# Performance work log

Measured on AMD Instinct MI355X. Metric: run time of the kernel, lower is better.

## Reference

```python
import jax, jax.numpy as jnp
import numpy as np

N, D = 50000, 1000
FH1, FH2 = 256, 128
GH1, GH2, H = 64, 30, 3
NC = 10
E = 800000
BN_EPS = 1e-5


def setup_inputs() -> dict:
    key = jax.random.key(0)
    ks = iter(jax.random.split(key, 48))
    nk = lambda: next(ks)
    r = lambda *s: jax.random.normal(nk(), s, jnp.float32) * 0.05
    g = lambda n: 1.0 + jax.random.normal(nk(), (n,), jnp.float32) * 0.01
    return dict(
        x=jax.random.normal(nk(), (N, D), jnp.float32),
        edge_index=jax.random.randint(nk(), (2, E), 0, N, dtype=jnp.int32),
        enc_w1=r(D, FH1), enc_b1=r(FH1), enc_g1=g(FH1), enc_bt1=r(FH1),
        enc_w2=r(FH1, FH2), enc_b2=r(FH2), enc_g2=g(FH2), enc_bt2=r(FH2),
        gat1_w=r(FH2, H * GH1), gat1_asrc=r(H, GH1), gat1_adst=r(H, GH1), gat1_b=r(H * GH1),
        gat2_w=r(H * GH1, GH2), gat2_asrc=r(1, GH2), gat2_adst=r(1, GH2), gat2_b=r(GH2),
        gat3_w=r(H * GH1, GH2), gat3_asrc=r(1, GH2), gat3_adst=r(1, GH2), gat3_b=r(GH2),
        dec_w1=r(GH2, FH2), dec_b1=r(FH2), dec_g1=g(FH2), dec_bt1=r(FH2),
        dec_w2=r(FH2, FH1), dec_b2=r(FH1), dec_g2=g(FH1), dec_bt2=r(FH1),
        dec_w3=r(FH1, D), dec_b3=r(D),
        clu_w1=r(GH2, FH2), clu_b1=r(FH2), clu_g1=g(FH2), clu_bt1=r(FH2),
        clu_w2=r(FH2, NC), clu_b2=r(NC),
    )


def _bn_elu(h, w, b, gm, bt):
    # Linear -> BatchNorm1d (batch stats) -> ELU; dropout is identity at eval
    h = h @ w + b
    m = h.mean(0)
    v = h.var(0)
    return jax.nn.elu(gm * (h - m) * jax.lax.rsqrt(v + BN_EPS) + bt)


def _gat(h, src, dst, n, w, a_src, a_dst, b, heads, oc, concat):
    # PyG GATConv: per-head linear, edge-wise LeakyReLU(0.2) scores,
    # softmax over incoming edges of each dst node, weighted scatter-sum.
    hh = (h @ w).reshape(n, heads, oc)            # [N,H,C]
    s_src = jnp.sum(hh * a_src, -1)               # [N,H]
    s_dst = jnp.sum(hh * a_dst, -1)               # [N,H]
    e = jax.nn.leaky_relu(s_src[src] + s_dst[dst], negative_slope=0.2)  # [E,H]
    m = jax.ops.segment_max(e, dst, num_segments=n)
    p = jnp.exp(e - m[dst])
    denom = jax.ops.segment_sum(p, dst, num_segments=n)
    alpha = p / denom[dst]                        # [E,H]
    msg = hh[src] * alpha[..., None]              # [E,H,C]
    out = jax.ops.segment_sum(msg, dst, num_segments=n)
    out = out.reshape(n, heads * oc) if concat else out.mean(1)
    return out + b


def reference(x, edge_index,
              enc_w1, enc_b1, enc_g1, enc_bt1, enc_w2, enc_b2, enc_g2, enc_bt2,
              gat1_w, gat1_asrc, gat1_adst, gat1_b,
              gat2_w, gat2_asrc, gat2_adst, gat2_b,
              gat3_w, gat3_asrc, gat3_adst, gat3_b,
              dec_w1, dec_b1, dec_g1, dec_bt1, dec_w2, dec_b2, dec_g2, dec_bt2, dec_w3, dec_b3,
              clu_w1, clu_b1, clu_g1, clu_bt1, clu_w2, clu_b2):
    n = x.shape[0]
    loops = jnp.arange(n, dtype=edge_index.dtype)  # GATConv add_self_loops=True
    src = jnp.concatenate([edge_index[0], loops])
    dst = jnp.concatenate([edge_index[1], loops])

    h = _bn_elu(x, enc_w1, enc_b1, enc_g1, enc_bt1)
    h = _bn_elu(h, enc_w2, enc_b2, enc_g2, enc_bt2)
    h = jax.nn.relu(_gat(h, src, dst, n, gat1_w, gat1_asrc, gat1_adst, gat1_b, H, GH1, True))
    mu = _gat(h, src, dst, n, gat2_w, gat2_asrc, gat2_adst, gat2_b, 1, GH2, False)
    logvar = _gat(h, src, dst, n, gat3_w, gat3_asrc, gat3_adst, gat3_b, 1, GH2, False)
    z = mu  # eval-mode reparameterize returns mu

    d = _bn_elu(z, dec_w1, dec_b1, dec_g1, dec_bt1)
    d = _bn_elu(d, dec_w2, dec_b2, dec_g2, dec_bt2)
    x_rec = d @ dec_w3 + dec_b3

    c = _bn_elu(z, clu_w1, clu_b1, clu_g1, clu_bt1)
    pred = jax.nn.softmax(c @ clu_w2 + clu_b2, axis=1)
    return (pred, x_rec, z, mu, logvar)
```

## Files before the change

### kernel.cpp

```cpp
#include <hip/hip_runtime.h>
#include <hip/hip_bf16.h>

typedef short short8 __attribute__((ext_vector_type(8)));
typedef short short4v __attribute__((ext_vector_type(4)));
typedef float f32x4 __attribute__((ext_vector_type(4)));

static __device__ __forceinline__ short f2bf(float f){
  __hip_bfloat16 h = __float2bfloat16(f);
  return __builtin_bit_cast(short, h);
}
static __device__ __forceinline__ float b2f(short s){
  unsigned int u = ((unsigned int)(unsigned short)s) << 16;
  return __builtin_bit_cast(float, u);
}
static __device__ __forceinline__ float lrelu(float x){ return x > 0.f ? x : 0.2f*x; }
static __device__ __forceinline__ float eluf(float x){ return x > 0.f ? x : (__expf(x)-1.f); }
static __device__ __forceinline__ int imin(int a,int b){ return a<b?a:b; }

typedef const __attribute__((address_space(1))) void as1_void;
typedef __attribute__((address_space(3))) void as3_void;
static __device__ __forceinline__ void gload16(const void* g, void* l){
  __builtin_amdgcn_global_load_lds((as1_void*)g, (as3_void*)l, 16, 0, 0);
}
template<int NN> __device__ __forceinline__ void wait_vm(){
  if constexpr (NN==0) asm volatile("s_waitcnt vmcnt(0)" ::: "memory");
  else if constexpr (NN==3) asm volatile("s_waitcnt vmcnt(3)" ::: "memory");
  else if constexpr (NN==4) asm volatile("s_waitcnt vmcnt(4)" ::: "memory");
  else if constexpr (NN==6) asm volatile("s_waitcnt vmcnt(6)" ::: "memory");
  else if constexpr (NN==8) asm volatile("s_waitcnt vmcnt(8)" ::: "memory");
}

__global__ __launch_bounds__(256) void cvt_x(const float* __restrict__ x, short* __restrict__ xb, int M){
  int row = blockIdx.x*2 + (threadIdx.x>>7);
  int c8  = (threadIdx.x&127)*8;
  if (row >= M || c8 >= 1000) return;
  const float* p = x + (size_t)row*1000 + c8;
  float4 f0 = *(const float4*)p, f1 = *(const float4*)(p+4);
  short8 o;
  o[0]=f2bf(f0.x);o[1]=f2bf(f0.y);o[2]=f2bf(f0.z);o[3]=f2bf(f0.w);
  o[4]=f2bf(f1.x);o[5]=f2bf(f1.y);o[6]=f2bf(f1.z);o[7]=f2bf(f1.w);
  *(short8*)&xb[(size_t)row*1000 + c8] = o;
}

template<int BN, bool OBF16, bool CSTATS>
__global__ __launch_bounds__(256) void gemm_g(
    const short* __restrict__ A, int lda, const short* __restrict__ Bt, int ldb,
    void* __restrict__ Cv, const float* __restrict__ bias,
    float* __restrict__ ssum, float* __restrict__ ssq,
    int M, int N, int K, int ldc)
{
  constexpr int BM = 128, BK = 32, GPR = 4;
  constexpr int WN = BN/2, FM = 4, FN = WN/16;
  constexpr int AI = (BM*GPR)/(4*64);
  constexpr int BI_T = (BN*GPR)/64;
  constexpr bool BDUP = (BI_T < 4);
  constexpr int BI = BDUP ? BI_T : BI_T/4;
  constexpr int LPT = AI + BI;
  constexpr int TS = (BM+BN)*BK;
  __shared__ short lds[4][TS];

  const int tid = threadIdx.x, wid = tid>>6, lane = tid&63;
  const int wm = wid>>1, wn = wid&1;
  const int bm = blockIdx.x*BM, bn = blockIdx.y*BN;
  const int lr = lane&15, lg = lane>>4;
  const int nt = (K + BK - 1)/BK;

  f32x4 acc[FM][FN] = {};

  auto STAGE = [&](int t){
    int buf = t & 3, k0 = t*BK;
    #pragma unroll
    for (int i=0;i<AI;i++){
      int ci = wid*AI + i;
      int c = ci*64 + lane;
      int row = c>>2, g = c&3;
      int gr = imin(bm+row, M-1);
      const short* src = A + (size_t)gr*lda + k0 + ((g ^ (row&3))<<3);
      gload16(src, &lds[buf][ci*512]);
    }
    #pragma unroll
    for (int i=0;i<BI;i++){
      int bi = BDUP ? i : wid*BI + i;
      int c = bi*64 + lane;
      int row = c>>2, g = c&3;
      const short* src = Bt + (size_t)(bn+row)*ldb + k0 + ((g ^ (row&3))<<3);
      gload16(src, &lds[buf][BM*BK + bi*512]);
    }
  };

  for (int s=0; s<3 && s<nt; ++s) STAGE(s);

  for (int t=0; t<nt; ++t){
    int newer = imin(nt, t+3) - t - 1;
    if (newer >= 2) wait_vm<2*LPT>();
    else if (newer == 1) wait_vm<LPT>();
    else wait_vm<0>();
    __builtin_amdgcn_s_barrier();
    __builtin_amdgcn_sched_barrier(0);
    if (t+3 < nt) STAGE(t+3);
    int buf = t & 3;
    short8 af[FM], bf[FN];
    #pragma unroll
    for (int m=0;m<FM;m++){
      int r = wm*64 + m*16 + lr;
      af[m] = *(short8*)&lds[buf][r*BK + ((lg ^ (r&3))<<3)];
    }
    #pragma unroll
    for (int n=0;n<FN;n++){
      int r = wn*WN + n*16 + lr;
      bf[n] = *(short8*)&lds[buf][BM*BK + r*BK + ((lg ^ (r&3))<<3)];
    }
    #pragma unroll
    for (int m=0;m<FM;m++)
      #pragma unroll
      for (int n=0;n<FN;n++)
        acc[m][n] = __builtin_amdgcn_mfma_f32_16x16x32_bf16(af[m], bf[n], acc[m][n], 0, 0, 0);
  }

  #pragma unroll
  for (int m=0;m<FM;m++)
    #pragma unroll
    for (int n=0;n<FN;n++)
      #pragma unroll
      for (int q=0;q<4;q++){
        int row = bm + wm*64 + m*16 + lg*4 + q;
        int col = bn + wn*WN + n*16 + lr;
        if (row < M && col < N){
          float v = acc[m][n][q];
          if (bias) v += bias[col];
          if (OBF16) ((short*)Cv)[(size_t)row*ldc + col] = f2bf(v);
          else       ((float*)Cv)[(size_t)row*ldc + col] = v;
        }
      }
  if (CSTATS){
    #pragma unroll
    for (int n=0;n<FN;n++){
      float s = 0.f, q2 = 0.f;
      #pragma unroll
      for (int m=0;m<FM;m++)
        #pragma unroll
        for (int q=0;q<4;q++){
          int row = bm + wm*64 + m*16 + lg*4 + q;
          if (row < M){ float v = acc[m][n][q]; s += v; q2 += v*v; }
        }
      s  += __shfl_xor(s, 16);  s += __shfl_xor(s, 32);
      q2 += __shfl_xor(q2, 16); q2 += __shfl_xor(q2, 32);
      if (lg == 0){
        int col = bn + wn*WN + n*16 + lr;
        atomicAdd(&ssum[col], s);
        atomicAdd(&ssq[col],  q2);
      }
    }
  }
}

struct WEnt { const float* src; short* dst; int K, N, KP, NR; };
struct WTab { WEnt e[10]; };
__global__ __launch_bounds__(256) void wtrans_all(WTab tab){
  WEnt w = tab.e[blockIdx.y];
  int gid = blockIdx.x*256 + threadIdx.x;
  if (gid >= w.NR * w.KP) return;
  int n = gid / w.KP, k = gid - n*w.KP;
  float v = (k < w.K && n < w.N) ? w.src[(size_t)k*w.N + n] : 0.f;
  w.dst[gid] = f2bf(v);
}

template<int C>
__global__ __launch_bounds__(256) void bn_elu_apply2(const float* __restrict__ H, short* __restrict__ O,
    int M, float invM,
    const float* __restrict__ ssum, const float* __restrict__ ssq,
    const float* __restrict__ g, const float* __restrict__ bt){
  __shared__ float sc[C], sh[C];
  for (int c = threadIdx.x; c < C; c += 256){
    float mn  = ssum[c]*invM;
    float var = ssq[c]*invM - mn*mn;
    float s = g[c]*rsqrtf(var + 1e-5f);
    sc[c] = s; sh[c] = bt[c] - mn*s;
  }
  __syncthreads();
  int total4 = M*(C/4);
  for (int i = blockIdx.x*256+threadIdx.x; i < total4; i += gridDim.x*256){
    float4 v = ((const float4*)H)[i];
    int cb = (i*4) & (C-1);
    short4v o;
    o[0] = f2bf(eluf(v.x*sc[cb+0]+sh[cb+0]));
    o[1] = f2bf(eluf(v.y*sc[cb+1]+sh[cb+1]));
    o[2] = f2bf(eluf(v.z*sc[cb+2]+sh[cb+2]));
    o[3] = f2bf(eluf(v.w*sc[cb+3]+sh[cb+3]));
    ((short4v*)O)[i] = o;
  }
}

__global__ __launch_bounds__(256) void bn_elu_split(const float* __restrict__ H,
    short* __restrict__ Od, short* __restrict__ Oc, int M, float invM,
    const float* __restrict__ ssum, const float* __restrict__ ssq,
    const float* __restrict__ gd, const float* __restrict__ btd,
    const float* __restrict__ gc, const float* __restrict__ btc){
  __shared__ float sc[256], sh[256];
  {
    int c = threadIdx.x;
    float mn  = ssum[c]*invM;
    float var = ssq[c]*invM - mn*mn;
    float gg = (c<128) ? gd[c] : gc[c-128];
    float bb = (c<128) ? btd[c] : btc[c-128];
    float s = gg*rsqrtf(var + 1e-5f);
    sc[c] = s; sh[c] = bb - mn*s;
  }
  __syncthreads();
  int total4 = M*64;
  for (int i = blockIdx.x*256+threadIdx.x; i < total4; i += gridDim.x*256){
    float4 v = ((const float4*)H)[i];
    int cb = (i*4) & 255;
    short4v o;
    o[0] = f2bf(eluf(v.x*sc[cb+0]+sh[cb+0]));
    o[1] = f2bf(eluf(v.y*sc[cb+1]+sh[cb+1]));
    o[2] = f2bf(eluf(v.z*sc[cb+2]+sh[cb+2]));
    o[3] = f2bf(eluf(v.w*sc[cb+3]+sh[cb+3]));
    int row = i>>6;
    short* O = (cb < 128) ? Od : Oc;
    *(short4v*)&O[(size_t)row*128 + (cb&127)] = o;
  }
}

__global__ void hist_kernel(const int* __restrict__ d, int E, int* __restrict__ deg){
  int i = blockIdx.x*256 + threadIdx.x;
  if (i < E) atomicAdd(&deg[d[i]], 1);
}
__global__ __launch_bounds__(256) void scan1(const int* __restrict__ deg, int* __restrict__ offs,
                                             int* __restrict__ bsum, int n){
  __shared__ int sm[256];
  int tid = threadIdx.x;
  int base = blockIdx.x*1024 + tid*4;
  int v0 = base+0<n ? deg[base+0] : 0;
  int v1 = base+1<n ? deg[base+1] : 0;
  int v2 = base+2<n ? deg[base+2] : 0;
  int v3 = base+3<n ? deg[base+3] : 0;
  int ts = v0+v1+v2+v3;
  sm[tid] = ts;
  __syncthreads();
  #pragma unroll
  for (int d=1; d<256; d<<=1){
    int t = (tid>=d) ? sm[tid-d] : 0;
    __syncthreads();
    sm[tid] += t;
    __syncthreads();
  }
  int ex = sm[tid] - ts;
  if (base+0<n) offs[base+0] = ex;
  if (base+1<n) offs[base+1] = ex+v0;
  if (base+2<n) offs[base+2] = ex+v0+v1;
  if (base+3<n) offs[base+3] = ex+v0+v1+v2;
  if (tid==255) bsum[blockIdx.x] = sm[255];
}
__global__ __launch_bounds__(256) void scan3(int* __restrict__ offs, const int* __restrict__ bsum,
                      int* __restrict__ cursor, int n, int total){
  __shared__ int base_sm;
  int tgt = blockIdx.x >> 2;
  if (threadIdx.x < 64){
    int j = threadIdx.x;
    int v = (j < tgt) ? bsum[j] : 0;
    #pragma unroll
    for (int d=32; d; d>>=1) v += __shfl_xor(v, d);
    if (j == 0) base_sm = v;
  }
  __syncthreads();
  int i = blockIdx.x*256 + threadIdx.x;
  if (i < n){ int v = offs[i] + base_sm; offs[i]=v; cursor[i]=v; }
  if (i == 0) offs[n] = total;
}
__global__ void scatter_kernel(const int* __restrict__ s, const int* __restrict__ d, int E,
                               int* __restrict__ cursor, int* __restrict__ csr){
  int i = blockIdx.x*256 + threadIdx.x;
  if (i < E){ int pos = atomicAdd(&cursor[d[i]], 1); csr[pos] = s[i]; }
}

__global__ __launch_bounds__(256) void gat1_scores_bf(const short* __restrict__ hh,
    const float* __restrict__ as, const float* __restrict__ ad,
    float* __restrict__ ss, float* __restrict__ sd, int n){
  int w = threadIdx.x >> 6, lane = threadIdx.x & 63;
  int row = blockIdx.x*4 + w;
  if (row >= n) return;
  const short* hr = hh + (size_t)row*192;
  float ps[3], pd[3];
  #pragma unroll
  for (int h=0; h<3; h++){
    float v = b2f(hr[h*64 + lane]);
    ps[h] = v * as[h*64+lane];
    pd[h] = v * ad[h*64+lane];
  }
  #pragma unroll
  for (int m=32; m; m>>=1){
    #pragma unroll
    for (int h=0;h<3;h++){ ps[h] += __shfl_xor(ps[h], m); pd[h] += __shfl_xor(pd[h], m); }
  }
  if (lane == 0){
    #pragma unroll
    for (int h=0;h<3;h++){ ss[row*3+h]=ps[h]; sd[row*3+h]=pd[h]; }
  }
}

__global__ __launch_bounds__(256) void gat1_gather_bf(const int* __restrict__ offs, const int* __restrict__ csr,
    const short* __restrict__ hh, const float* __restrict__ ss, const float* __restrict__ sd,
    const float* __restrict__ bias, short* __restrict__ out, int n){
  int w = threadIdx.x >> 6, lane = threadIdx.x & 63;
  int dst = blockIdx.x*4 + w;
  if (dst >= n) return;
  float sd0 = sd[dst*3+0], sd1 = sd[dst*3+1], sd2 = sd[dst*3+2];
  float p0 = __expf(lrelu(ss[dst*3+0]+sd0));
  float p1 = __expf(lrelu(ss[dst*3+1]+sd1));
  float p2 = __expf(lrelu(ss[dst*3+2]+sd2));
  const short* hr = hh + (size_t)dst*192;
  float a0 = p0*b2f(hr[lane]), a1 = p1*b2f(hr[64+lane]), a2 = p2*b2f(hr[128+lane]);
  float d0 = p0, d1 = p1, d2 = p2;
  int p = offs[dst], pe = offs[dst+1];
  for (; p+4 <= pe; p += 4){
    int s0=csr[p], s1=csr[p+1], s2=csr[p+2], s3=csr[p+3];
    float e00=ss[s0*3+0], e01=ss[s0*3+1], e02=ss[s0*3+2];
    float e10=ss[s1*3+0], e11=ss[s1*3+1], e12=ss[s1*3+2];
    float e20=ss[s2*3+0], e21=ss[s2*3+1], e22=ss[s2*3+2];
    float e30=ss[s3*3+0], e31=ss[s3*3+1], e32=ss[s3*3+2];
    const short* r0 = hh + (size_t)s0*192;
    const short* r1 = hh + (size_t)s1*192;
    const short* r2 = hh + (size_t)s2*192;
    const short* r3 = hh + (size_t)s3*192;
    float v00=b2f(r0[lane]), v01=b2f(r0[64+lane]), v02=b2f(r0[128+lane]);
    float v10=b2f(r1[lane]), v11=b2f(r1[64+lane]), v12=b2f(r1[128+lane]);
    float v20=b2f(r2[lane]), v21=b2f(r2[64+lane]), v22=b2f(r2[128+lane]);
    float v30=b2f(r3[lane]), v31=b2f(r3[64+lane]), v32=b2f(r3[128+lane]);
    float q00=__expf(lrelu(e00+sd0)), q01=__expf(lrelu(e01+sd1)), q02=__expf(lrelu(e02+sd2));
    float q10=__expf(lrelu(e10+sd0)), q11=__expf(lrelu(e11+sd1)), q12=__expf(lrelu(e12+sd2));
    float q20=__expf(lrelu(e20+sd0)), q21=__expf(lrelu(e21+sd1)), q22=__expf(lrelu(e22+sd2));
    float q30=__expf(lrelu(e30+sd0)), q31=__expf(lrelu(e31+sd1)), q32=__expf(lrelu(e32+sd2));
    a0 += q00*v00 + q10*v10 + q20*v20 + q30*v30;
    a1 += q01*v01 + q11*v11 + q21*v21 + q31*v31;
    a2 += q02*v02 + q12*v12 + q22*v22 + q32*v32;
    d0 += q00+q10+q20+q30;
    d1 += q01+q11+q21+q31;
    d2 += q02+q12+q22+q32;
  }
  for (; p < pe; ++p){
    int src = csr[p];
    float q0 = __expf(lrelu(ss[src*3+0]+sd0));
    float q1 = __expf(lrelu(ss[src*3+1]+sd1));
    float q2 = __expf(lrelu(ss[src*3+2]+sd2));
    const short* sr = hh + (size_t)src*192;
    a0 += q0*b2f(sr[lane]); a1 += q1*b2f(sr[64+lane]); a2 += q2*b2f(sr[128+lane]);
    d0 += q0; d1 += q1; d2 += q2;
  }
  float v0 = a0/d0 + bias[lane];
  float v1 = a1/d1 + bias[64+lane];
  float v2 = a2/d2 + bias[128+lane];
  short* orow = out + (size_t)dst*192;
  orow[lane]      = f2bf(v0 > 0.f ? v0 : 0.f);
  orow[64+lane]   = f2bf(v1 > 0.f ? v1 : 0.f);
  orow[128+lane]  = f2bf(v2 > 0.f ? v2 : 0.f);
}

__global__ __launch_bounds__(256) void gat23_scores(const float* __restrict__ hh23,
    const float* __restrict__ a2s, const float* __restrict__ a2d,
    const float* __restrict__ a3s, const float* __restrict__ a3d,
    float* __restrict__ s2s, float* __restrict__ s2d, float* __restrict__ s3s, float* __restrict__ s3d, int n){
  int w = threadIdx.x >> 6, lane = threadIdx.x & 63;
  int row = blockIdx.x*4 + w;
  if (row >= n) return;
  float p[4] = {0.f,0.f,0.f,0.f};
  if (lane < 30){
    float v2 = hh23[(size_t)row*64+lane], v3 = hh23[(size_t)row*64+32+lane];
    p[0]=v2*a2s[lane]; p[1]=v2*a2d[lane]; p[2]=v3*a3s[lane]; p[3]=v3*a3d[lane];
  }
  #pragma unroll
  for (int m=32; m; m>>=1){
    #pragma unroll
    for (int j=0;j<4;j++) p[j] += __shfl_xor(p[j], m);
  }
  if (lane == 0){ s2s[row]=p[0]; s2d[row]=p[1]; s3s[row]=p[2]; s3d[row]=p[3]; }
}

__global__ __launch_bounds__(256) void gat23_gather(const int* __restrict__ offs, const int* __restrict__ csr,
    const float* __restrict__ hh23,
    const float* __restrict__ s2s, const float* __restrict__ s2d,
    const float* __restrict__ s3s, const float* __restrict__ s3d,
    const float* __restrict__ b2, const float* __restrict__ b3,
    float* __restrict__ zs, float* __restrict__ mus, float* __restrict__ lvs,
    short* __restrict__ zbf, int n){
  int w = threadIdx.x >> 6, lane = threadIdx.x & 63;
  int dst = blockIdx.x*4 + w;
  if (dst >= n) return;
  bool lo = lane < 32;
  int c = lane & 31;
  bool valid = c < 30;
  float sdA = s2d[dst], sdB = s3d[dst];
  float sdx = lo ? sdA : sdB;
  const float* ssx = lo ? s2s : s3s;
  float p2 = __expf(lrelu(s2s[dst]+sdA));
  float p3 = __expf(lrelu(s3s[dst]+sdB));
  float val = valid ? hh23[(size_t)dst*64+lane] : 0.f;
  float acc = (lo ? p2 : p3) * val;
  float den2 = p2, den3 = p3;
  int p = offs[dst], pe = offs[dst+1];
  for (; p+4 <= pe; p += 4){
    int s0=csr[p], s1=csr[p+1], s2i=csr[p+2], s3i=csr[p+3];
    float eA0=ssx[s0], eA1=ssx[s1], eA2=ssx[s2i], eA3=ssx[s3i];
    float f20=s2s[s0], f21=s2s[s1], f22=s2s[s2i], f23=s2s[s3i];
    float f30=s3s[s0], f31=s3s[s1], f32=s3s[s2i], f33=s3s[s3i];
    float v0 = valid ? hh23[(size_t)s0*64+lane] : 0.f;
    float v1 = valid ? hh23[(size_t)s1*64+lane] : 0.f;
    float v2 = valid ? hh23[(size_t)s2i*64+lane] : 0.f;
    float v3 = valid ? hh23[(size_t)s3i*64+lane] : 0.f;
    float qx0=__expf(lrelu(eA0+sdx)), qx1=__expf(lrelu(eA1+sdx));
    float qx2=__expf(lrelu(eA2+sdx)), qx3=__expf(lrelu(eA3+sdx));
    acc += qx0*v0 + qx1*v1 + qx2*v2 + qx3*v3;
    den2 += __expf(lrelu(f20+sdA)) + __expf(lrelu(f21+sdA)) + __expf(lrelu(f22+sdA)) + __expf(lrelu(f23+sdA));
    den3 += __expf(lrelu(f30+sdB)) + __expf(lrelu(f31+sdB)) + __expf(lrelu(f32+sdB)) + __expf(lrelu(f33+sdB));
  }
  for (; p < pe; ++p){
    int src = csr[p];
    float q2 = __expf(lrelu(s2s[src]+sdA));
    float q3 = __expf(lrelu(s3s[src]+sdB));
    float v = valid ? hh23[(size_t)src*64+lane] : 0.f;
    acc += (lo ? q2 : q3) * v;
    den2 += q2; den3 += q3;
  }
  if (lo){
    if (valid){
      float v = acc/den2 + b2[c];
      zs[(size_t)dst*30+c]  = v;
      mus[(size_t)dst*30+c] = v;
      zbf[(size_t)dst*32+c] = f2bf(v);
    } else {
      zbf[(size_t)dst*32+c] = 0;
    }
  } else if (valid){
    lvs[(size_t)dst*30+c] = acc/den3 + b3[c];
  }
}

__global__ __launch_bounds__(256) void softmax10(const float* __restrict__ in, float* __restrict__ out, int n){
  int row = blockIdx.x*256 + threadIdx.x;
  if (row >= n) return;
  const float* r = in + (size_t)row*10;
  float m = r[0];
  #pragma unroll
  for (int j=1;j<10;j++) m = fmaxf(m, r[j]);
  float e[10], s = 0.f;
  #pragma unroll
  for (int j=0;j<10;j++){ e[j] = __expf(r[j]-m); s += e[j]; }
  float inv = 1.f/s;
  float* o = out + (size_t)row*10;
  #pragma unroll
  for (int j=0;j<10;j++) o[j] = e[j]*inv;
}

static inline int cdiv(int a, int b){ return (a + b - 1) / b; }

extern "C" void kernel_launch(void* const* d_in, const int* in_sizes, int n_in,
                              void* d_out, int out_size, void* d_ws, size_t ws_size,
                              hipStream_t stream)
{
  const float* x        = (const float*)d_in[0];
  const int*   ei       = (const int*)  d_in[1];
  const float* enc_w1   = (const float*)d_in[2];
  const float* enc_g1   = (const float*)d_in[4];
  const float* enc_bt1  = (const float*)d_in[5];
  const float* enc_w2   = (const float*)d_in[6];
  const float* enc_g2   = (const float*)d_in[8];
  const float* enc_bt2  = (const float*)d_in[9];
  const float* gat1_w   = (const float*)d_in[10];
  const float* gat1_as  = (const float*)d_in[11];
  const float* gat1_ad  = (const float*)d_in[12];
  const float* gat1_b   = (const float*)d_in[13];
  const float* gat2_w   = (const float*)d_in[14];
  const float* gat2_as  = (const float*)d_in[15];
  const float* gat2_ad  = (const float*)d_in[16];
  const float* gat2_b   = (const float*)d_in[17];
  const float* gat3_w   = (const float*)d_in[18];
  const float* gat3_as  = (const float*)d_in[19];
  const float* gat3_ad  = (const float*)d_in[20];
  const float* gat3_b   = (const float*)d_in[21];
  const float* dec_w1   = (const float*)d_in[22];
  const float* dec_g1   = (const float*)d_in[24];
  const float* dec_bt1  = (const float*)d_in[25];
  const float* dec_w2   = (const float*)d_in[26];
  const float* dec_g2   = (const float*)d_in[28];
  const float* dec_bt2  = (const float*)d_in[29];
  const float* dec_w3   = (const float*)d_in[30];
  const float* dec_b3   = (const float*)d_in[31];
  const float* clu_w1   = (const float*)d_in[32];
  const float* clu_g1   = (const float*)d_in[34];
  const float* clu_bt1  = (const float*)d_in[35];
  const float* clu_w2   = (const float*)d_in[36];
  const float* clu_b2   = (const float*)d_in[37];

  const int N = in_sizes[0] / 1000;
  const int E = in_sizes[1] / 2;
  const int* e_src = ei;
  const int* e_dst = ei + E;
  const float invN = 1.f/(float)N;

  float* out  = (float*)d_out;
  float* pred = out;
  float* xrec = out + (size_t)N*10;
  float* zs   = xrec + (size_t)N*1000;
  float* mus  = zs  + (size_t)N*30;
  float* lvs  = mus + (size_t)N*30;

  char* ws = (char*)d_ws;
  size_t off = 0;
  auto alloc = [&](size_t bytes)->char*{
    char* p = ws + off;
    off = (off + bytes + 255) & ~(size_t)255;
    return p;
  };
  short* t_enc1  = (short*)alloc(256*1024*2);
  short* t_enc2  = (short*)alloc(128*256*2);
  short* t_gat1  = (short*)alloc(192*128*2);
  short* t_gat23 = (short*)alloc(64*192*2);
  short* t_dc1   = (short*)alloc(256*32*2);
  short* t_dec2  = (short*)alloc(256*128*2);
  short* t_dec3  = (short*)alloc(1024*256*2);
  short* t_clu2  = (short*)alloc(32*128*2);
  float* h1f  = (float*)alloc((size_t)N*256*4);
  short* h1b  = (short*)alloc((size_t)N*256*2);
  float* h2f  = (float*)alloc((size_t)N*128*4);
  short* h2b  = (short*)alloc((size_t)N*128*2);
  short* hh1b = (short*)alloc((size_t)N*192*2);
  short* h3b  = (short*)alloc((size_t)N*192*2);
  float* hh23f= (float*)alloc((size_t)N*64*4);
  short* zbf  = (short*)alloc((size_t)N*32*2);
  float* ss1  = (float*)alloc((size_t)N*3*4);
  float* sd1  = (float*)alloc((size_t)N*3*4);
  float* s2s  = (float*)alloc((size_t)N*4);
  float* s2d  = (float*)alloc((size_t)N*4);
  float* s3s  = (float*)alloc((size_t)N*4);
  float* s3d  = (float*)alloc((size_t)N*4);
  float* stats= (float*)alloc(2048*4);
  int*   deg  = (int*)alloc((size_t)(N+1)*4);
  int*   offs = (int*)alloc((size_t)(N+1)*4);
  int*   curp = (int*)alloc((size_t)(N+1)*4);
  int*   bsum = (int*)alloc(256*4);
  int*   csr  = (int*)alloc((size_t)E*4);
  short* xb   = h1b;
  float* dc1f = h2f;
  short* d1b  = h3b;
  short* c1b  = (short*)hh23f;
  float* d2f  = h1f;
  short* d2b  = h1b;
  float* c2   = (float*)zbf;
  float* st_enc1 = stats, *st_enc2 = stats+512, *st_dc1 = stats+768, *st_dec2 = stats+1280;

  WTab tab;
  tab.e[0] = {enc_w1, t_enc1, 1000, 256, 1024, 256};
  tab.e[1] = {enc_w2, t_enc2, 256, 128, 256, 128};
  tab.e[2] = {gat1_w, t_gat1, 128, 192, 128, 192};
  tab.e[3] = {gat2_w, t_gat23, 192, 30, 192, 32};
  tab.e[4] = {gat3_w, t_gat23 + 32*192, 192, 30, 192, 32};
  tab.e[5] = {dec_w1, t_dc1, 30, 128, 32, 128};
  tab.e[6] = {clu_w1, t_dc1 + 128*32, 30, 128, 32, 128};
  tab.e[7] = {dec_w2, t_dec2, 128, 256, 128, 256};
  tab.e[8] = {dec_w3, t_dec3, 256, 1000, 256, 1024};
  tab.e[9] = {clu_w2, t_clu2, 128, 10, 128, 32};
  wtrans_all<<<dim3(1024, 10), 256, 0, stream>>>(tab);
  hipMemsetAsync(stats, 0, 2048*4, stream);
  hipMemsetAsync(deg, 0, (size_t)(N+1)*4, stream);

  hist_kernel<<<cdiv(E,256), 256, 0, stream>>>(e_dst, E, deg);
  int nb = cdiv(N, 1024);
  scan1<<<nb, 256, 0, stream>>>(deg, offs, bsum, N);
  scan3<<<cdiv(N,256), 256, 0, stream>>>(offs, bsum, curp, N, E);
  scatter_kernel<<<cdiv(E,256), 256, 0, stream>>>(e_src, e_dst, E, curp, csr);

  const int MB = cdiv(N, 128);

  cvt_x<<<cdiv(N,2), 256, 0, stream>>>(x, xb, N);
  gemm_g<128,false,true><<<dim3(MB,2), 256, 0, stream>>>(xb, 1000, t_enc1, 1024, h1f, nullptr, st_enc1, st_enc1+256, N, 256, 1000, 256);
  bn_elu_apply2<256><<<2048, 256, 0, stream>>>(h1f, h1b, N, invN, st_enc1, st_enc1+256, enc_g1, enc_bt1);

  gemm_g<128,false,true><<<dim3(MB,1), 256, 0, stream>>>(h1b, 256, t_enc2, 256, h2f, nullptr, st_enc2, st_enc2+128, N, 128, 256, 128);
  bn_elu_apply2<128><<<2048, 256, 0, stream>>>(h2f, h2b, N, invN, st_enc2, st_enc2+128, enc_g2, enc_bt2);

  gemm_g<64,true,false><<<dim3(MB,3), 256, 0, stream>>>(h2b, 128, t_gat1, 128, hh1b, nullptr, nullptr, nullptr, N, 192, 128, 192);
  gat1_scores_bf<<<cdiv(N,4), 256, 0, stream>>>(hh1b, gat1_as, gat1_ad, ss1, sd1, N);
  gat1_gather_bf<<<cdiv(N,4), 256, 0, stream>>>(offs, csr, hh1b, ss1, sd1, gat1_b, h3b, N);

  gemm_g<64,false,false><<<dim3(MB,1), 256, 0, stream>>>(h3b, 192, t_gat23, 192, hh23f, nullptr, nullptr, nullptr, N, 64, 192, 64);
  gat23_scores<<<cdiv(N,4), 256, 0, stream>>>(hh23f, gat2_as, gat2_ad, gat3_as, gat3_ad, s2s, s2d, s3s, s3d, N);
  gat23_gather<<<cdiv(N,4), 256, 0, stream>>>(offs, csr, hh23f, s2s, s2d, s3s, s3d, gat2_b, gat3_b, zs, mus, lvs, zbf, N);

  gemm_g<128,false,true><<<dim3(MB,2), 256, 0, stream>>>(zbf, 32, t_dc1, 32, dc1f, nullptr, st_dc1, st_dc1+256, N, 256, 32, 256);
  bn_elu_split<<<2048, 256, 0, stream>>>(dc1f, d1b, c1b, N, invN, st_dc1, st_dc1+256, dec_g1, dec_bt1, clu_g1, clu_bt1);

  gemm_g<128,false,true><<<dim3(MB,2), 256, 0, stream>>>(d1b, 128, t_dec2, 128, d2f, nullptr, st_dec2, st_dec2+256, N, 256, 128, 256);
  bn_elu_apply2<256><<<2048, 256, 0, stream>>>(d2f, d2b, N, invN, st_dec2, st_dec2+256, dec_g2, dec_bt2);

  gemm_g<128,false,false><<<dim3(MB,8), 256, 0, stream>>>(d2b, 256, t_dec3, 256, xrec, dec_b3, nullptr, nullptr, N, 1000, 256, 1000);

  gemm_g<32,false,false><<<dim3(MB,1), 256, 0, stream>>>(c1b, 128, t_clu2, 128, c2, clu_b2, nullptr, nullptr, N, 10, 128, 10);
  softmax10<<<cdiv(N,256), 256, 0, stream>>>(c2, pred, N);
}
```

Baseline: 701.5 us.

## Halve GEMM row tile, fuse GAT2/3 scores and softmax into GEMM epilogues

Templates the GEMM on BM and switches every GEMM to 64-row tiles, doubling the number of blocks. The GAT2/3 attention-score reduction and the final 10-class softmax now run inside GEMM epilogues, which removes two kernel launches and an intermediate round trip. The CSR index loads in both gather kernels are software-prefetched one iteration ahead. Smaller tiles add more B-tile reloads and change the vmcnt wait counts, which now depend on the new per-thread load count.

```diff
diff --git a/kernel.cpp b/kernel.cpp
--- a/kernel.cpp
+++ b/kernel.cpp
@@ -24,10 +24,13 @@
 }
 template<int NN> __device__ __forceinline__ void wait_vm(){
   if constexpr (NN==0) asm volatile("s_waitcnt vmcnt(0)" ::: "memory");
+  else if constexpr (NN==1) asm volatile("s_waitcnt vmcnt(1)" ::: "memory");
+  else if constexpr (NN==2) asm volatile("s_waitcnt vmcnt(2)" ::: "memory");
   else if constexpr (NN==3) asm volatile("s_waitcnt vmcnt(3)" ::: "memory");
   else if constexpr (NN==4) asm volatile("s_waitcnt vmcnt(4)" ::: "memory");
   else if constexpr (NN==6) asm volatile("s_waitcnt vmcnt(6)" ::: "memory");
   else if constexpr (NN==8) asm volatile("s_waitcnt vmcnt(8)" ::: "memory");
+  else asm volatile("s_waitcnt vmcnt(0)" ::: "memory");
 }
 
 __global__ __launch_bounds__(256) void cvt_x(const float* __restrict__ x, short* __restrict__ xb, int M){
@@ -42,15 +45,20 @@
   *(short8*)&xb[(size_t)row*1000 + c8] = o;
 }
 
-template<int BN, bool OBF16, bool CSTATS>
+template<int BM, int BN, bool OBF16, bool CST, bool SMAX, bool G23S>
 __global__ __launch_bounds__(256) void gemm_g(
     const short* __restrict__ A, int lda, const short* __restrict__ Bt, int ldb,
-    void* __restrict__ Cv, const float* __restrict__ bias,
-    float* __restrict__ ssum, float* __restrict__ ssq,
-    int M, int N, int K, int ldc)
+    void* __restrict__ Cv, int ldc, const float* __restrict__ bias,
+    int M, int N, int K,
+    float* __restrict__ o_sum, float* __restrict__ o_sq,
+    float* __restrict__ s2s, float* __restrict__ s2d,
+    float* __restrict__ s3s, float* __restrict__ s3d,
+    const float* __restrict__ a2s, const float* __restrict__ a2d,
+    const float* __restrict__ a3s, const float* __restrict__ a3d)
 {
-  constexpr int BM = 128, BK = 32, GPR = 4;
-  constexpr int WN = BN/2, FM = 4, FN = WN/16;
+  constexpr int BK = 32, GPR = 4;
+  constexpr int WM = BM/2, WN = BN/2;
+  constexpr int FM = WM/16, FN = WN/16;
   constexpr int AI = (BM*GPR)/(4*64);
   constexpr int BI_T = (BN*GPR)/64;
   constexpr bool BDUP = (BI_T < 4);
@@ -102,7 +110,7 @@
     short8 af[FM], bf[FN];
     #pragma unroll
     for (int m=0;m<FM;m++){
-      int r = wm*64 + m*16 + lr;
+      int r = wm*WM + m*16 + lr;
       af[m] = *(short8*)&lds[buf][r*BK + ((lg ^ (r&3))<<3)];
     }
     #pragma unroll
@@ -117,13 +125,33 @@
         acc[m][n] = __builtin_amdgcn_mfma_f32_16x16x32_bf16(af[m], bf[n], acc[m][n], 0, 0, 0);
   }
 
+  if (SMAX){
+    #pragma unroll
+    for (int m=0;m<FM;m++)
+      #pragma unroll
+      for (int q=0;q<4;q++){
+        int row = bm + wm*WM + m*16 + lg*4 + q;
+        float v = (lr < 10) ? (acc[m][0][q] + bias[lr]) : -3e38f;
+        float mx = v;
+        #pragma unroll
+        for (int d=1; d<16; d<<=1) mx = fmaxf(mx, __shfl_xor(mx, d));
+        float e = (lr < 10) ? __expf(v - mx) : 0.f;
+        float sm = e;
+        #pragma unroll
+        for (int d=1; d<16; d<<=1) sm += __shfl_xor(sm, d);
+        if (wn == 0 && lr < 10 && row < M)
+          ((float*)Cv)[(size_t)row*10 + lr] = e/sm;
+      }
+    return;
+  }
+
   #pragma unroll
   for (int m=0;m<FM;m++)
     #pragma unroll
     for (int n=0;n<FN;n++)
       #pragma unroll
       for (int q=0;q<4;q++){
-        int row = bm + wm*64 + m*16 + lg*4 + q;
+        int row = bm + wm*WM + m*16 + lg*4 + q;
         int col = bn + wn*WN + n*16 + lr;
         if (row < M && col < N){
           float v = acc[m][n][q];
@@ -132,7 +160,34 @@
           else       ((float*)Cv)[(size_t)row*ldc + col] = v;
         }
       }
-  if (CSTATS){
+
+  if (G23S){
+    float a_s[FN], a_d[FN];
+    #pragma unroll
+    for (int n=0;n<FN;n++){
+      int cl = n*16 + lr;
+      bool valid = cl < 30;
+      a_s[n] = valid ? (wn ? a3s[cl] : a2s[cl]) : 0.f;
+      a_d[n] = valid ? (wn ? a3d[cl] : a2d[cl]) : 0.f;
+    }
+    #pragma unroll
+    for (int m=0;m<FM;m++)
+      #pragma unroll
+      for (int q=0;q<4;q++){
+        int row = bm + wm*WM + m*16 + lg*4 + q;
+        float ps = 0.f, pd = 0.f;
+        #pragma unroll
+        for (int n=0;n<FN;n++){ ps += acc[m][n][q]*a_s[n]; pd += acc[m][n][q]*a_d[n]; }
+        #pragma unroll
+        for (int d=1; d<16; d<<=1){ ps += __shfl_xor(ps, d); pd += __shfl_xor(pd, d); }
+        if (lr == 0 && row < M){
+          if (wn){ s3s[row] = ps; s3d[row] = pd; }
+          else   { s2s[row] = ps; s2d[row] = pd; }
+        }
+      }
+  }
+
+  if (CST){
     #pragma unroll
     for (int n=0;n<FN;n++){
       float s = 0.f, q2 = 0.f;
@@ -140,22 +195,21 @@
       for (int m=0;m<FM;m++)
         #pragma unroll
         for (int q=0;q<4;q++){
-          int row = bm + wm*64 + m*16 + lg*4 + q;
+          int row = bm + wm*WM + m*16 + lg*4 + q;
           if (row < M){ float v = acc[m][n][q]; s += v; q2 += v*v; }
         }
       s  += __shfl_xor(s, 16);  s += __shfl_xor(s, 32);
       q2 += __shfl_xor(q2, 16); q2 += __shfl_xor(q2, 32);
       if (lg == 0){
         int col = bn + wn*WN + n*16 + lr;
-        atomicAdd(&ssum[col], s);
-        atomicAdd(&ssq[col],  q2);
+        if (col < N){ atomicAdd(&o_sum[col], s); atomicAdd(&o_sq[col], q2); }
       }
     }
   }
 }
 
 struct WEnt { const float* src; short* dst; int K, N, KP, NR; };
-struct WTab { WEnt e[10]; };
+struct WTab { WEnt e[12]; };
 __global__ __launch_bounds__(256) void wtrans_all(WTab tab){
   WEnt w = tab.e[blockIdx.y];
   int gid = blockIdx.x*256 + threadIdx.x;
@@ -313,8 +367,12 @@
   float a0 = p0*b2f(hr[lane]), a1 = p1*b2f(hr[64+lane]), a2 = p2*b2f(hr[128+lane]);
   float d0 = p0, d1 = p1, d2 = p2;
   int p = offs[dst], pe = offs[dst+1];
-  for (; p+4 <= pe; p += 4){
-    int s0=csr[p], s1=csr[p+1], s2=csr[p+2], s3=csr[p+3];
+  int n0=0,n1=0,n2=0,n3=0;
+  if (p+4 <= pe){ n0=csr[p]; n1=csr[p+1]; n2=csr[p+2]; n3=csr[p+3]; }
+  while (p+4 <= pe){
+    int s0=n0, s1=n1, s2=n2, s3=n3;
+    int pn = p+4;
+    if (pn+4 <= pe){ n0=csr[pn]; n1=csr[pn+1]; n2=csr[pn+2]; n3=csr[pn+3]; }
     float e00=ss[s0*3+0], e01=ss[s0*3+1], e02=ss[s0*3+2];
     float e10=ss[s1*3+0], e11=ss[s1*3+1], e12=ss[s1*3+2];
     float e20=ss[s2*3+0], e21=ss[s2*3+1], e22=ss[s2*3+2];
@@ -337,6 +395,7 @@
     d0 += q00+q10+q20+q30;
     d1 += q01+q11+q21+q31;
     d2 += q02+q12+q22+q32;
+    p = pn;
   }
   for (; p < pe; ++p){
     int src = csr[p];
@@ -354,26 +413,6 @@
   orow[lane]      = f2bf(v0 > 0.f ? v0 : 0.f);
   orow[64+lane]   = f2bf(v1 > 0.f ? v1 : 0.f);
   orow[128+lane]  = f2bf(v2 > 0.f ? v2 : 0.f);
-}
-
-__global__ __launch_bounds__(256) void gat23_scores(const float* __restrict__ hh23,
-    const float* __restrict__ a2s, const float* __restrict__ a2d,
-    const float* __restrict__ a3s, const float* __restrict__ a3d,
-    float* __restrict__ s2s, float* __restrict__ s2d, float* __restrict__ s3s, float* __restrict__ s3d, int n){
-  int w = threadIdx.x >> 6, lane = threadIdx.x & 63;
-  int row = blockIdx.x*4 + w;
-  if (row >= n) return;
-  float p[4] = {0.f,0.f,0.f,0.f};
-  if (lane < 30){
-    float v2 = hh23[(size_t)row*64+lane], v3 = hh23[(size_t)row*64+32+lane];
-    p[0]=v2*a2s[lane]; p[1]=v2*a2d[lane]; p[2]=v3*a3s[lane]; p[3]=v3*a3d[lane];
-  }
-  #pragma unroll
-  for (int m=32; m; m>>=1){
-    #pragma unroll
-    for (int j=0;j<4;j++) p[j] += __shfl_xor(p[j], m);
-  }
-  if (lane == 0){ s2s[row]=p[0]; s2d[row]=p[1]; s3s[row]=p[2]; s3d[row]=p[3]; }
 }
 
 __global__ __launch_bounds__(256) void gat23_gather(const int* __restrict__ offs, const int* __restrict__ csr,
@@ -398,8 +437,12 @@
   float acc = (lo ? p2 : p3) * val;
   float den2 = p2, den3 = p3;
   int p = offs[dst], pe = offs[dst+1];
-  for (; p+4 <= pe; p += 4){
-    int s0=csr[p], s1=csr[p+1], s2i=csr[p+2], s3i=csr[p+3];
+  int n0=0,n1=0,n2=0,n3=0;
+  if (p+4 <= pe){ n0=csr[p]; n1=csr[p+1]; n2=csr[p+2]; n3=csr[p+3]; }
+  while (p+4 <= pe){
+    int s0=n0, s1=n1, s2i=n2, s3i=n3;
+    int pn = p+4;
+    if (pn+4 <= pe){ n0=csr[pn]; n1=csr[pn+1]; n2=csr[pn+2]; n3=csr[pn+3]; }
     float eA0=ssx[s0], eA1=ssx[s1], eA2=ssx[s2i], eA3=ssx[s3i];
     float f20=s2s[s0], f21=s2s[s1], f22=s2s[s2i], f23=s2s[s3i];
     float f30=s3s[s0], f31=s3s[s1], f32=s3s[s2i], f33=s3s[s3i];
@@ -412,6 +455,7 @@
     acc += qx0*v0 + qx1*v1 + qx2*v2 + qx3*v3;
     den2 += __expf(lrelu(f20+sdA)) + __expf(lrelu(f21+sdA)) + __expf(lrelu(f22+sdA)) + __expf(lrelu(f23+sdA));
     den3 += __expf(lrelu(f30+sdB)) + __expf(lrelu(f31+sdB)) + __expf(lrelu(f32+sdB)) + __expf(lrelu(f33+sdB));
+    p = pn;
   }
   for (; p < pe; ++p){
     int src = csr[p];
@@ -433,22 +477,6 @@
   } else if (valid){
     lvs[(size_t)dst*30+c] = acc/den3 + b3[c];
   }
-}
-
-__global__ __launch_bounds__(256) void softmax10(const float* __restrict__ in, float* __restrict__ out, int n){
-  int row = blockIdx.x*256 + threadIdx.x;
-  if (row >= n) return;
-  const float* r = in + (size_t)row*10;
-  float m = r[0];
-  #pragma unroll
-  for (int j=1;j<10;j++) m = fmaxf(m, r[j]);
-  float e[10], s = 0.f;
-  #pragma unroll
-  for (int j=0;j<10;j++){ e[j] = __expf(r[j]-m); s += e[j]; }
-  float inv = 1.f/s;
-  float* o = out + (size_t)row*10;
-  #pragma unroll
-  for (int j=0;j<10;j++) o[j] = e[j]*inv;
 }
 
 static inline int cdiv(int a, int b){ return (a + b - 1) / b; }
@@ -513,7 +541,7 @@
   };
   short* t_enc1  = (short*)alloc(256*1024*2);
   short* t_enc2  = (short*)alloc(128*256*2);
-  short* t_gat1  = (short*)alloc(192*128*2);
+  short* t_gat1  = (short*)alloc(256*128*2);
   short* t_gat23 = (short*)alloc(64*192*2);
   short* t_dc1   = (short*)alloc(256*32*2);
   short* t_dec2  = (short*)alloc(256*128*2);
@@ -545,21 +573,22 @@
   short* c1b  = (short*)hh23f;
   float* d2f  = h1f;
   short* d2b  = h1b;
-  float* c2   = (float*)zbf;
   float* st_enc1 = stats, *st_enc2 = stats+512, *st_dc1 = stats+768, *st_dec2 = stats+1280;
 
   WTab tab;
-  tab.e[0] = {enc_w1, t_enc1, 1000, 256, 1024, 256};
-  tab.e[1] = {enc_w2, t_enc2, 256, 128, 256, 128};
-  tab.e[2] = {gat1_w, t_gat1, 128, 192, 128, 192};
-  tab.e[3] = {gat2_w, t_gat23, 192, 30, 192, 32};
-  tab.e[4] = {gat3_w, t_gat23 + 32*192, 192, 30, 192, 32};
-  tab.e[5] = {dec_w1, t_dc1, 30, 128, 32, 128};
-  tab.e[6] = {clu_w1, t_dc1 + 128*32, 30, 128, 32, 128};
-  tab.e[7] = {dec_w2, t_dec2, 128, 256, 128, 256};
-  tab.e[8] = {dec_w3, t_dec3, 256, 1000, 256, 1024};
-  tab.e[9] = {clu_w2, t_clu2, 128, 10, 128, 32};
-  wtrans_all<<<dim3(1024, 10), 256, 0, stream>>>(tab);
+  tab.e[0]  = {enc_w1, t_enc1, 1000, 256, 1024, 256};
+  tab.e[1]  = {enc_w2, t_enc2, 256, 128, 256, 128};
+  tab.e[2]  = {gat1_w, t_gat1, 128, 192, 128, 256};
+  tab.e[3]  = {gat2_w, t_gat23, 192, 30, 192, 32};
+  tab.e[4]  = {gat3_w, t_gat23 + 32*192, 192, 30, 192, 32};
+  tab.e[5]  = {dec_w1, t_dc1, 30, 128, 32, 128};
+  tab.e[6]  = {clu_w1, t_dc1 + 128*32, 30, 128, 32, 128};
+  tab.e[7]  = {dec_w2, t_dec2, 128, 256, 128, 256};
+  tab.e[8]  = {dec_w3, t_dec3, 256, 1000, 256, 1024};
+  tab.e[9]  = {clu_w2, t_clu2, 128, 10, 128, 32};
+  tab.e[10] = {enc_w1, t_enc1, 0, 0, 0, 0};
+  tab.e[11] = {enc_w1, t_enc1, 0, 0, 0, 0};
+  wtrans_all<<<dim3(1024, 12), 256, 0, stream>>>(tab);
   hipMemsetAsync(stats, 0, 2048*4, stream);
   hipMemsetAsync(deg, 0, (size_t)(N+1)*4, stream);
 
@@ -569,31 +598,45 @@
   scan3<<<cdiv(N,256), 256, 0, stream>>>(offs, bsum, curp, N, E);
   scatter_kernel<<<cdiv(E,256), 256, 0, stream>>>(e_src, e_dst, E, curp, csr);
 
-  const int MB = cdiv(N, 128);
+  const int MB = cdiv(N, 64);
 
   cvt_x<<<cdiv(N,2), 256, 0, stream>>>(x, xb, N);
-  gemm_g<128,false,true><<<dim3(MB,2), 256, 0, stream>>>(xb, 1000, t_enc1, 1024, h1f, nullptr, st_enc1, st_enc1+256, N, 256, 1000, 256);
+  gemm_g<64,128,false,true,false,false><<<dim3(MB,2), 256, 0, stream>>>(
+      xb, 1000, t_enc1, 1024, h1f, 256, nullptr, N, 256, 1000,
+      st_enc1, st_enc1+256, nullptr,nullptr,nullptr,nullptr, nullptr,nullptr,nullptr,nullptr);
   bn_elu_apply2<256><<<2048, 256, 0, stream>>>(h1f, h1b, N, invN, st_enc1, st_enc1+256, enc_g1, enc_bt1);
 
-  gemm_g<128,false,true><<<dim3(MB,1), 256, 0, stream>>>(h1b, 256, t_enc2, 256, h2f, nullptr, st_enc2, st_enc2+128, N, 128, 256, 128);
+  gemm_g<64,128,false,true,false,false><<<dim3(MB,1), 256, 0, stream>>>(
+      h1b, 256, t_enc2, 256, h2f, 128, nullptr, N, 128, 256,
+      st_enc2, st_enc2+128, nullptr,nullptr,nullptr,nullptr, nullptr,nullptr,nullptr,nullptr);
   bn_elu_apply2<128><<<2048, 256, 0, stream>>>(h2f, h2b, N, invN, st_enc2, st_enc2+128, enc_g2, enc_bt2);
 
-  gemm_g<64,true,false><<<dim3(MB,3), 256, 0, stream>>>(h2b, 128, t_gat1, 128, hh1b, nullptr, nullptr, nullptr, N, 192, 128, 192);
+  gemm_g<64,64,true,false,false,false><<<dim3(MB,3), 256, 0, stream>>>(
+      h2b, 128, t_gat1, 128, hh1b, 192, nullptr, N, 192, 128,
+      nullptr,nullptr, nullptr,nullptr,nullptr,nullptr, nullptr,nullptr,nullptr,nullptr);
   gat1_scores_bf<<<cdiv(N,4), 256, 0, stream>>>(hh1b, gat1_as, gat1_ad, ss1, sd1, N);
   gat1_gather_bf<<<cdiv(N,4), 256, 0, stream>>>(offs, csr, hh1b, ss1, sd1, gat1_b, h3b, N);
 
-  gemm_g<64,false,false><<<dim3(MB,1), 256, 0, stream>>>(h3b, 192, t_gat23, 192, hh23f, nullptr, nullptr, nullptr, N, 64, 192, 64);
-  gat23_scores<<<cdiv(N,4), 256, 0, stream>>>(hh23f, gat2_as, gat2_ad, gat3_as, gat3_ad, s2s, s2d, s3s, s3d, N);
+  gemm_g<64,64,false,false,false,true><<<dim3(MB,1), 256, 0, stream>>>(
+      h3b, 192, t_gat23, 192, hh23f, 64, nullptr, N, 64, 192,
+      nullptr,nullptr, s2s,s2d,s3s,s3d, gat2_as,gat2_ad,gat3_as,gat3_ad);
   gat23_gather<<<cdiv(N,4), 256, 0, stream>>>(offs, csr, hh23f, s2s, s2d, s3s, s3d, gat2_b, gat3_b, zs, mus, lvs, zbf, N);
 
-  gemm_g<128,false,true><<<dim3(MB,2), 256, 0, stream>>>(zbf, 32, t_dc1, 32, dc1f, nullptr, st_dc1, st_dc1+256, N, 256, 32, 256);
+  gemm_g<64,128,false,true,false,false><<<dim3(MB,2), 256, 0, stream>>>(
+      zbf, 32, t_dc1, 32, dc1f, 256, nullptr, N, 256, 32,
+      st_dc1, st_dc1+256, nullptr,nullptr,nullptr,nullptr, nullptr,nullptr,nullptr,nullptr);
   bn_elu_split<<<2048, 256, 0, stream>>>(dc1f, d1b, c1b, N, invN, st_dc1, st_dc1+256, dec_g1, dec_bt1, clu_g1, clu_bt1);
 
-  gemm_g<128,false,true><<<dim3(MB,2), 256, 0, stream>>>(d1b, 128, t_dec2, 128, d2f, nullptr, st_dec2, st_dec2+256, N, 256, 128, 256);
+  gemm_g<64,128,false,true,false,false><<<dim3(MB,2), 256, 0, stream>>>(
+      d1b, 128, t_dec2, 128, d2f, 256, nullptr, N, 256, 128,
+      st_dec2, st_dec2+256, nullptr,nullptr,nullptr,nullptr, nullptr,nullptr,nullptr,nullptr);
   bn_elu_apply2<256><<<2048, 256, 0, stream>>>(d2f, d2b, N, invN, st_dec2, st_dec2+256, dec_g2, dec_bt2);
 
-  gemm_g<128,false,false><<<dim3(MB,8), 256, 0, stream>>>(d2b, 256, t_dec3, 256, xrec, dec_b3, nullptr, nullptr, N, 1000, 256, 1000);
-
-  gemm_g<32,false,false><<<dim3(MB,1), 256, 0, stream>>>(c1b, 128, t_clu2, 128, c2, clu_b2, nullptr, nullptr, N, 10, 128, 10);
-  softmax10<<<cdiv(N,256), 256, 0, stream>>>(c2, pred, N);
-}
+  gemm_g<64,128,false,false,false,false><<<dim3(MB,8), 256, 0, stream>>>(
+      d2b, 256, t_dec3, 256, xrec, 1000, dec_b3, N, 1000, 256,
+      nullptr,nullptr, nullptr,nullptr,nullptr,nullptr, nullptr,nullptr,nullptr,nullptr);
+
+  gemm_g<64,32,false,false,true,false><<<dim3(MB,1), 256, 0, stream>>>(
+      c1b, 128, t_clu2, 128, pred, 10, clu_b2, N, 10, 128,
+      nullptr,nullptr, nullptr,nullptr,nullptr,nullptr, nullptr,nullptr,nullptr,nullptr);
+}
```

Result: slower. 795.9 us (+13.5%).
